# Optimization experiments

Hardware: AMD Instinct MI355X
Metric: run time of the kernel (lower is better)

Reference implementation:

```python
import jax, jax.numpy as jnp
import numpy as np

HEADS = 6
WSIZE = 8
SHIFTS = 4
EPS = 1e-5


def conv1x1(x, w, b=None):
    # x: (B,C,H,W), w: (O,C)
    y = jnp.einsum('bchw,oc->bohw', x, w)
    if b is not None:
        y = y + b[None, :, None, None]
    return y


def spatial_shift(x):
    # ShiftConv2d1 depthwise fixed-kernel conv == per-group spatial shift with zero pad
    C = x.shape[1]
    g = C // 5
    x0, x1, x2, x3, x4 = (x[:, :g], x[:, g:2 * g], x[:, 2 * g:3 * g],
                          x[:, 3 * g:4 * g], x[:, 4 * g:])
    left = jnp.pad(x0[:, :, :, 1:], ((0, 0), (0, 0), (0, 0), (0, 1)))   # kernel (1,2)
    right = jnp.pad(x1[:, :, :, :-1], ((0, 0), (0, 0), (0, 0), (1, 0)))  # kernel (1,0)
    up = jnp.pad(x2[:, :, 1:, :], ((0, 0), (0, 0), (0, 1), (0, 0)))      # kernel (2,1)
    down = jnp.pad(x3[:, :, :-1, :], ((0, 0), (0, 0), (1, 0), (0, 0)))   # kernel (0,1)
    return jnp.concatenate([left, right, up, down, x4], axis=1)


def window_attn(xb, ws, heads, shifts):
    # xb: (B, 2*heads*c, H, W); self-similarity attention q@q^T (no separate K, no scaling)
    if shifts > 0:
        xb = jnp.roll(xb, (-(ws // 2), -(ws // 2)), axis=(2, 3))
    b, c2, H, W = xb.shape
    cd = c2 // (2 * heads)
    nh, nw = H // ws, W // ws
    t = xb.reshape(b, 2, heads, cd, nh, ws, nw, ws)
    t = t.transpose(1, 0, 4, 6, 2, 5, 7, 3).reshape(2, b * nh * nw, heads, ws * ws, cd)
    q, v = t[0], t[1]
    atn = jax.nn.softmax(jnp.einsum('whnc,whmc->whnm', q, q), axis=-1)
    o = jnp.einsum('whnm,whmc->whnc', atn, v)
    o = o.reshape(b, nh, nw, heads, ws, ws, cd)
    o = o.transpose(0, 3, 6, 1, 4, 2, 5).reshape(b, heads * cd, H, W)
    if shifts > 0:
        o = jnp.roll(o, (ws // 2, ws // 2), axis=(2, 3))
    return o


def setup_inputs() -> dict:
    key = jax.random.key(0)
    ks = jax.random.split(key, 8)
    B, C, H, W = 2, 180, 256, 256
    s = 0.05
    return {
        'x': jax.random.normal(ks[0], (B, C, H, W), jnp.float32),
        'w0': jax.random.normal(ks[1], (2 * C, C), jnp.float32) * s,
        'b0': jnp.zeros((2 * C,), jnp.float32),
        'w1': jax.random.normal(ks[2], (C, 2 * C), jnp.float32) * s,
        'b1': jnp.zeros((C,), jnp.float32),
        'w_in': jax.random.normal(ks[3], (2 * C, C), jnp.float32) * s,
        'b_in': jnp.zeros((2 * C,), jnp.float32),
        'bn_g': jnp.ones((2 * C,), jnp.float32),
        'bn_b': jnp.zeros((2 * C,), jnp.float32),
        'w_out': jax.random.normal(ks[4], (C, C), jnp.float32) * s,
        'b_out': jnp.zeros((C,), jnp.float32),
    }


def reference(x, w0, b0, w1, b1, w_in, b_in, bn_g, bn_b, w_out, b_out):
    # --- LFE (shift-conv FFN), exp_ratio=2, relu ---
    y = conv1x1(spatial_shift(x), w0, b0)
    y = jax.nn.relu(y)
    y = conv1x1(spatial_shift(y), w1, b1)
    x = y + x
    # --- GMSA (3 parallel shifted-window self-similarity attentions) ---
    z = conv1x1(x, w_in, b_in)
    mu = z.mean(axis=(0, 2, 3), keepdims=True)
    var = z.var(axis=(0, 2, 3), keepdims=True)  # biased, matching BN training forward
    z = (z - mu) / jnp.sqrt(var + EPS) * bn_g[None, :, None, None] + bn_b[None, :, None, None]
    cs = z.shape[1] // 3
    sizes = [WSIZE // 4, WSIZE // 2, WSIZE]
    outs = [window_attn(z[:, i * cs:(i + 1) * cs], sizes[i], HEADS, SHIFTS)
            for i in range(3)]
    out = conv1x1(jnp.concatenate(outs, axis=1), w_out, b_out)
    return out + x
```

## Files before the change

kernel.cpp:

```cpp
#include <hip/hip_runtime.h>
#include <hip/hip_bf16.h>

#define HWSZ 65536
#define NPIX 131072

typedef unsigned short u16;
typedef __bf16 bf16x8 __attribute__((ext_vector_type(8)));
typedef float f32x4 __attribute__((ext_vector_type(4)));
typedef unsigned short u16x2 __attribute__((ext_vector_type(2)));
typedef unsigned short u16x4 __attribute__((ext_vector_type(4)));
typedef unsigned short u16x8 __attribute__((ext_vector_type(8)));
typedef unsigned short u16x8u __attribute__((ext_vector_type(8), aligned(4)));

__device__ inline u16 f2bf(float f) {
    unsigned int x = __builtin_bit_cast(unsigned int, f);
    unsigned int r = x + 0x7FFFu + ((x >> 16) & 1u);
    return (u16)(r >> 16);
}
__device__ inline float bf2f(u16 u) {
    unsigned int x = ((unsigned int)u) << 16;
    return __builtin_bit_cast(float, x);
}

__global__ __launch_bounds__(256) void prep_w(
    const float* __restrict__ w0, const float* __restrict__ w1,
    const float* __restrict__ wi, const float* __restrict__ wo,
    u16* __restrict__ W0p, u16* __restrict__ W1p,
    u16* __restrict__ Wip, u16* __restrict__ Wop)
{
    const int i = blockIdx.x * 256 + threadIdx.x;
    {
        const int r = i / 192, c = i % 192;
        const bool ok = (r < 360) && (c < 180);
        W0p[i] = ok ? f2bf(w0[r * 180 + c]) : (u16)0;
        Wip[i] = ok ? f2bf(wi[r * 180 + c]) : (u16)0;
    }
    {
        const int r = i / 384, c = i % 384;
        W1p[i] = (r < 180 && c < 360) ? f2bf(w1[r * 360 + c]) : (u16)0;
    }
    if (i < 36864) {
        const int r = i / 192, c = i % 192;
        Wop[i] = (r < 180 && c < 180) ? f2bf(wo[r * 180 + c]) : (u16)0;
    }
}

template<int CI, int CO, int G, int INM, int XSTR, bool RELU, int RES, int OUTM, int OSTR, bool COSPLIT>
__global__ __launch_bounds__(256, 4) void conv_v9(
    const void* __restrict__ Xv, const u16* __restrict__ Wp,
    const float* __restrict__ bias, const void* __restrict__ Rv,
    void* __restrict__ Yv)
{
    constexpr int CI_PAD = ((CI + 31) / 32) * 32;
    constexpr int NSTEP  = CI_PAD / 32;
    constexpr int LDK    = 40;

    __shared__ u16 Xt[2][64 * LDK];

    const int tid = threadIdx.x;
    const int bid = blockIdx.x;
    int px_tile, co0;
    if (COSPLIT) {
        co0     = ((bid >> 3) & 1) * 192;
        px_tile = ((bid >> 4) << 3) | (bid & 7);
    } else {
        co0 = blockIdx.y * 192; px_tile = bid;
    }
    const int p0   = px_tile << 6;
    const int b    = p0 >> 16;
    const int pix0 = p0 & 65535;
    const int h    = pix0 >> 8;
    const int w0c  = pix0 & 255;
    const int lane = tid & 63, wid = tid >> 6;
    const int lr = lane & 15, lg = lane >> 4;
    const int co_wave = co0 + wid * 48;

    const float* Xf = (const float*)Xv + (size_t)b * CI * HWSZ;
    const u16*   Xh = (const u16*)Xv;

    const int xn  = tid & 63;
    const int k4a = tid >> 6;

    auto loadX = [&](int kt, u16x4 (&r)[2]) {
        #pragma unroll
        for (int it = 0; it < 2; ++it) {
            const int k4 = k4a + it * 4;
            const int c0 = kt + k4 * 4;
            u16x4 v = {0, 0, 0, 0};
            if (c0 < CI) {
                int dh = 0, dw = 0;
                if (G > 0) {
                    const int g = c0 / G;
                    if      (g == 0) dw = 1;
                    else if (g == 1) dw = -1;
                    else if (g == 2) dh = 1;
                    else if (g == 3) dh = -1;
                }
                const int hh = h + dh;
                const int wp = w0c + xn + dw;
                if (hh >= 0 && hh < 256 && wp >= 0 && wp < 256) {
                    if constexpr (INM == 1) {
                        v = *(const u16x4*)&Xh[(size_t)((b << 16) | (hh << 8) | wp) * XSTR + c0];
                    } else {
                        const float* xs = Xf + (size_t)c0 * HWSZ + hh * 256 + wp;
                        #pragma unroll
                        for (int j = 0; j < 4; ++j) v[j] = f2bf(xs[(size_t)j * HWSZ]);
                    }
                }
            }
            r[it] = v;
        }
    };

    auto loadW = [&](int kt, bf16x8 (&a)[3]) {
        #pragma unroll
        for (int mf = 0; mf < 3; ++mf)
            a[mf] = *(const bf16x8*)&Wp[(size_t)(co_wave + mf * 16 + lr) * CI_PAD + kt + lg * 8];
    };

    auto writeLDS = [&](u16x4 (&r)[2], int buf) {
        *(u16x4*)&Xt[buf][xn * LDK + k4a * 4]       = r[0];
        *(u16x4*)&Xt[buf][xn * LDK + (k4a + 4) * 4] = r[1];
    };

    f32x4 acc[3][4] = {};
    u16x4 raw[2][2];
    bf16x8 af[2][3];

    loadX(0, raw[0]);
    loadW(0, af[0]);
    writeLDS(raw[0], 0);

    #pragma unroll
    for (int s = 0; s < NSTEP; ++s) {
        const int cur = s & 1, nxt = cur ^ 1;
        __syncthreads();
        if (s + 1 < NSTEP) {
            loadX((s + 1) * 32, raw[nxt]);
            loadW((s + 1) * 32, af[nxt]);
        }
        bf16x8 bfr[4];
        #pragma unroll
        for (int nf = 0; nf < 4; ++nf)
            bfr[nf] = *(const bf16x8*)&Xt[cur][(nf * 16 + lr) * LDK + lg * 8];
        #pragma unroll
        for (int mf = 0; mf < 3; ++mf)
            #pragma unroll
            for (int nf = 0; nf < 4; ++nf)
                acc[mf][nf] = __builtin_amdgcn_mfma_f32_16x16x32_bf16(
                    af[cur][mf], bfr[nf], acc[mf][nf], 0, 0, 0);
        if (s + 1 < NSTEP) writeLDS(raw[nxt], nxt);
    }

    const float* Rf = (const float*)Rv;
    const u16*   Rh = (const u16*)Rv;
    #pragma unroll
    for (int mf = 0; mf < 3; ++mf) {
        const int co_b = co_wave + mf * 16 + lg * 4;
        if (co_b >= CO) continue;
        #pragma unroll
        for (int nf = 0; nf < 4; ++nf) {
            const int pl = pix0 + nf * 16 + lr;
            const size_t pg = (size_t)p0 + nf * 16 + lr;
            float v[4];
            #pragma unroll
            for (int r = 0; r < 4; ++r) {
                v[r] = acc[mf][nf][r] + bias[co_b + r];
                if (RELU) v[r] = fmaxf(v[r], 0.f);
            }
            if (RES == 1) {
                #pragma unroll
                for (int r = 0; r < 4; ++r)
                    v[r] += Rf[((size_t)(b * CO + co_b + r)) * HWSZ + pl];
            }
            if (RES == 2) {
                u16x4 rr = *(const u16x4*)&Rh[pg * 180 + co_b];
                #pragma unroll
                for (int r = 0; r < 4; ++r) v[r] += bf2f(rr[r]);
            }
            if (OUTM == 1) {
                u16x4 o;
                #pragma unroll
                for (int r = 0; r < 4; ++r) o[r] = f2bf(v[r]);
                *(u16x4*)&((u16*)Yv)[pg * OSTR + co_b] = o;
            } else {
                #pragma unroll
                for (int r = 0; r < 4; ++r)
                    ((float*)Yv)[((size_t)(b * CO + co_b + r)) * HWSZ + pl] = v[r];
            }
        }
    }
}

template<int CI, int CO, int G, int XSTR, bool RELU, int RES, int OUTM, int OSTR, bool COSPLIT>
__global__ __launch_bounds__(256) void conv_v10(
    const u16* __restrict__ Xh, const u16* __restrict__ Wp,
    const float* __restrict__ bias, const void* __restrict__ Rv,
    void* __restrict__ Yv)
{
    constexpr int CI_PAD = ((CI + 31) / 32) * 32;
    constexpr int NSTEP  = CI_PAD / 32;

    __shared__ u16 Xt[2][256 * 8];

    const int tid = threadIdx.x;
    const int bid = blockIdx.x;
    int px_tile, co0;
    if (COSPLIT) {
        co0     = ((bid >> 3) & 1) * 192;
        px_tile = ((bid >> 4) << 3) | (bid & 7);
    } else {
        co0 = blockIdx.y * 192; px_tile = bid;
    }
    const int p0   = px_tile << 6;
    const int b    = p0 >> 16;
    const int pix0 = p0 & 65535;
    const int h    = pix0 >> 8;
    const int w0c  = pix0 & 255;
    const int lane = tid & 63, wid = tid >> 6;
    const int lr = lane & 15, lg = lane >> 4;
    const int co_wave = co0 + wid * 48;

    const int sg  = (wid << 6) | lane;
    const int spx = sg >> 2;
    const int khp = sg & 3;
    const int kh  = khp ^ ((spx >> 1) & 3);

    auto stage = [&](int kt, int buf) {
        const int c0 = kt + kh * 8;
        u16* ldst_lane = &Xt[buf][sg * 8];
        int dh = 0, dw = 0; bool uni = true;
        if (G > 0) {
            const int g0 = c0 / G;
            uni = (g0 == (c0 + 7) / G);
            if      (g0 == 0) dw = 1;
            else if (g0 == 1) dw = -1;
            else if (g0 == 2) dh = 1;
            else if (g0 == 3) dh = -1;
        }
        const int hh = h + dh, wp = w0c + spx + dw;
        const bool pxok = (hh >= 0 && hh < 256 && wp >= 0 && wp < 256);
        if (c0 < CI && uni && pxok) {
            const u16* src = &Xh[(size_t)((b << 16) | (hh << 8) | wp) * XSTR + c0];
            u16* wbase = &Xt[buf][(wid << 6) * 8];
            __builtin_amdgcn_global_load_lds(
                (const __attribute__((address_space(1))) unsigned int*)src,
                (__attribute__((address_space(3))) unsigned int*)wbase, 16, 0, 0);
        } else {
            u16x8 t = {0, 0, 0, 0, 0, 0, 0, 0};
            if (c0 < CI && pxok) {
                #pragma unroll
                for (int j = 0; j < 8; ++j) {
                    const int c = c0 + j;
                    if (c < CI) {
                        int dh2 = 0, dw2 = 0;
                        if (G > 0) {
                            const int g = c / G;
                            if      (g == 0) dw2 = 1;
                            else if (g == 1) dw2 = -1;
                            else if (g == 2) dh2 = 1;
                            else if (g == 3) dh2 = -1;
                        }
                        const int h2 = h + dh2, w2 = w0c + spx + dw2;
                        if (h2 >= 0 && h2 < 256 && w2 >= 0 && w2 < 256)
                            t[j] = Xh[(size_t)((b << 16) | (h2 << 8) | w2) * XSTR + c];
                    }
                }
            }
            *(u16x8*)ldst_lane = t;
        }
    };

    auto loadW = [&](int kt, bf16x8 (&a)[3]) {
        #pragma unroll
        for (int mf = 0; mf < 3; ++mf)
            a[mf] = *(const bf16x8*)&Wp[(size_t)(co_wave + mf * 16 + lr) * CI_PAD + kt + lg * 8];
    };

    f32x4 acc[3][4] = {};
    bf16x8 af[2][3];

    stage(0, 0);
    loadW(0, af[0]);
    __syncthreads();

    #pragma unroll
    for (int s = 0; s < NSTEP; ++s) {
        const int cur = s & 1, nxt = cur ^ 1;
        if (s + 1 < NSTEP) {
            stage((s + 1) * 32, nxt);
            loadW((s + 1) * 32, af[nxt]);
        }
        bf16x8 bfr[4];
        #pragma unroll
        for (int nf = 0; nf < 4; ++nf) {
            const int pxr = nf * 16 + lr;
            const int kpp = lg ^ ((pxr >> 1) & 3);
            bfr[nf] = *(const bf16x8*)&Xt[cur][pxr * 32 + kpp * 8];
        }
        #pragma unroll
        for (int mf = 0; mf < 3; ++mf)
            #pragma unroll
            for (int nf = 0; nf < 4; ++nf)
                acc[mf][nf] = __builtin_amdgcn_mfma_f32_16x16x32_bf16(
                    af[cur][mf], bfr[nf], acc[mf][nf], 0, 0, 0);
        __syncthreads();
    }

    const float* Rf = (const float*)Rv;
    const u16*   Rh = (const u16*)Rv;
    #pragma unroll
    for (int mf = 0; mf < 3; ++mf) {
        const int co_b = co_wave + mf * 16 + lg * 4;
        if (co_b >= CO) continue;
        #pragma unroll
        for (int nf = 0; nf < 4; ++nf) {
            const int pl = pix0 + nf * 16 + lr;
            const size_t pg = (size_t)p0 + nf * 16 + lr;
            float v[4];
            #pragma unroll
            for (int r = 0; r < 4; ++r) {
                v[r] = acc[mf][nf][r] + bias[co_b + r];
                if (RELU) v[r] = fmaxf(v[r], 0.f);
            }
            if (RES == 1) {
                #pragma unroll
                for (int r = 0; r < 4; ++r)
                    v[r] += Rf[((size_t)(b * CO + co_b + r)) * HWSZ + pl];
            }
            if (RES == 2) {
                u16x4 rr = *(const u16x4*)&Rh[pg * 180 + co_b];
                #pragma unroll
                for (int r = 0; r < 4; ++r) v[r] += bf2f(rr[r]);
            }
            if (OUTM == 1) {
                u16x4 o;
                #pragma unroll
                for (int r = 0; r < 4; ++r) o[r] = f2bf(v[r]);
                *(u16x4*)&((u16*)Yv)[pg * OSTR + co_b] = o;
            } else {
                #pragma unroll
                for (int r = 0; r < 4; ++r)
                    ((float*)Yv)[((size_t)(b * CO + co_b + r)) * HWSZ + pl] = v[r];
            }
        }
    }
}

__global__ __launch_bounds__(256) void bn_part(const u16* __restrict__ zt,
                                               float* __restrict__ part)
{
    const int tid = threadIdx.x;
    const int oc  = tid & 63;
    const int pp  = tid >> 6;
    if (oc >= 45) return;
    const int stripe = blockIdx.x * 4 + pp;
    const int pb = blockIdx.x * 1024 + pp;
    float s[8] = {}, q[8] = {};
    for (int i = 0; i < 256; ++i) {
        const int p = pb + i * 4;
        u16x8 t = *(const u16x8*)&zt[(size_t)p * 360 + oc * 8];
        #pragma unroll
        for (int j = 0; j < 8; ++j) {
            float v = bf2f(t[j]);
            s[j] += v; q[j] += v * v;
        }
    }
    float* pr = part + ((size_t)stripe * 45 + oc) * 16;
    #pragma unroll
    for (int j = 0; j < 8; ++j) { pr[j] = s[j]; pr[8 + j] = q[j]; }
}

__global__ __launch_bounds__(256) void bn_fin(const float* __restrict__ part,
                                              const float* __restrict__ g,
                                              const float* __restrict__ bb,
                                              float* __restrict__ sc,
                                              float* __restrict__ sh)
{
    const int oc = blockIdx.x;
    const int t  = threadIdx.x;
    const float* p1 = part + ((size_t)t * 45 + oc) * 16;
    const float* p2 = part + ((size_t)(t + 256) * 45 + oc) * 16;
    float v[16];
    #pragma unroll
    for (int k = 0; k < 16; ++k) v[k] = p1[k] + p2[k];
    #pragma unroll
    for (int k = 0; k < 16; ++k)
        for (int m = 32; m; m >>= 1) v[k] += __shfl_xor(v[k], m, 64);
    __shared__ float red[4][16];
    if ((t & 63) == 0) {
        #pragma unroll
        for (int k = 0; k < 16; ++k) red[t >> 6][k] = v[k];
    }
    __syncthreads();
    if (t == 0) {
        const float invN = 1.f / (float)NPIX;
        #pragma unroll
        for (int j = 0; j < 8; ++j) {
            const int c = oc * 8 + j;
            float su = red[0][j] + red[1][j] + red[2][j] + red[3][j];
            float sq = red[0][8+j] + red[1][8+j] + red[2][8+j] + red[3][8+j];
            float mean = su * invN;
            float var  = sq * invN - mean * mean;
            float istd = 1.f / sqrtf(var + 1e-5f);
            float s = g[c] * istd;
            sc[c] = s;
            sh[c] = bb[c] - mean * s;
        }
    }
}

template<int WS>
__global__ __launch_bounds__(256) void attn_v3(
    const u16* __restrict__ zt, const float* __restrict__ scale,
    const float* __restrict__ shiftc, u16* __restrict__ ot, int chunk)
{
    constexpr int NP  = WS * WS;
    constexpr int GPB = 256 / NP;
    constexpr int SH  = WS / 2;
    constexpr int NW  = 256 / WS;

    __shared__ float qs[256 * 12];
    __shared__ float vs[256 * 12];
    __shared__ float scs[120], shs[120];

    const int tid = threadIdx.x;
    if (tid < 120) {
        scs[tid] = scale[chunk * 120 + tid];
        shs[tid] = shiftc[chunk * 120 + tid];
    }

    const int lg  = tid / NP;
    const int n   = tid % NP;
    const int gidx = blockIdx.x * GPB + lg;

    const int head = gidx % 6;
    const int win  = gidx / 6;
    const int wcol = win % NW;
    const int tmp  = win / NW;
    const int wrow = tmp % NW;
    const int b    = tmp / NW;

    const int i = n / WS, j = n % WS;
    const int hh = (wrow * WS + i + SH) & 255;
    const int ww = (wcol * WS + j + SH) & 255;
    const size_t zrow = (size_t)((b << 16) | (hh << 8) | ww) * 360;

    const int cq = chunk * 120 + head * 10;
    const int cl = head * 10;

    u16x8u q8 = *(const u16x8u*)&zt[zrow + cq];
    u16x2  q2 = *(const u16x2*)&zt[zrow + cq + 8];
    u16x8u v8 = *(const u16x8u*)&zt[zrow + cq + 60];
    u16x2  v2 = *(const u16x2*)&zt[zrow + cq + 68];
    __syncthreads();

    float q[10];
    float* qrow = &qs[tid * 12];
    float* vrow = &vs[tid * 12];
    #pragma unroll
    for (int c = 0; c < 8; ++c) {
        q[c] = bf2f(q8[c]) * scs[cl + c] + shs[cl + c];
        qrow[c] = q[c];
        vrow[c] = bf2f(v8[c]) * scs[60 + cl + c] + shs[60 + cl + c];
    }
    q[8] = bf2f(q2[0]) * scs[cl + 8] + shs[cl + 8];
    q[9] = bf2f(q2[1]) * scs[cl + 9] + shs[cl + 9];
    qrow[8] = q[8]; qrow[9] = q[9];
    vrow[8] = bf2f(v2[0]) * scs[60 + cl + 8] + shs[60 + cl + 8];
    vrow[9] = bf2f(v2[1]) * scs[60 + cl + 9] + shs[60 + cl + 9];
    qrow[10] = 0.f; qrow[11] = 0.f;
    vrow[10] = 0.f; vrow[11] = 0.f;
    __syncthreads();

    const float* qg = &qs[(lg * NP) * 12];
    const float* vg = &vs[(lg * NP) * 12];

    float mx = -1e30f;
    for (int m = 0; m < NP; ++m) {
        f32x4 a0 = *(const f32x4*)&qg[m * 12];
        f32x4 a1 = *(const f32x4*)&qg[m * 12 + 4];
        f32x4 a2 = *(const f32x4*)&qg[m * 12 + 8];
        float d = q[0]*a0[0] + q[1]*a0[1] + q[2]*a0[2] + q[3]*a0[3]
                + q[4]*a1[0] + q[5]*a1[1] + q[6]*a1[2] + q[7]*a1[3]
                + q[8]*a2[0] + q[9]*a2[1];
        mx = fmaxf(mx, d);
    }
    float s = 0.f;
    float o[10] = {};
    for (int m = 0; m < NP; ++m) {
        f32x4 a0 = *(const f32x4*)&qg[m * 12];
        f32x4 a1 = *(const f32x4*)&qg[m * 12 + 4];
        f32x4 a2 = *(const f32x4*)&qg[m * 12 + 8];
        float d = q[0]*a0[0] + q[1]*a0[1] + q[2]*a0[2] + q[3]*a0[3]
                + q[4]*a1[0] + q[5]*a1[1] + q[6]*a1[2] + q[7]*a1[3]
                + q[8]*a2[0] + q[9]*a2[1];
        float e = __expf(d - mx);
        s += e;
        f32x4 b0 = *(const f32x4*)&vg[m * 12];
        f32x4 b1 = *(const f32x4*)&vg[m * 12 + 4];
        f32x4 b2 = *(const f32x4*)&vg[m * 12 + 8];
        o[0] += e * b0[0]; o[1] += e * b0[1]; o[2] += e * b0[2]; o[3] += e * b0[3];
        o[4] += e * b1[0]; o[5] += e * b1[1]; o[6] += e * b1[2]; o[7] += e * b1[3];
        o[8] += e * b2[0]; o[9] += e * b2[1];
    }
    const float inv = 1.f / s;
    u16* orow = ot + (size_t)((b << 16) | (hh << 8) | ww) * 180 + chunk * 60 + head * 10;
    u16x8u o8;
    #pragma unroll
    for (int c = 0; c < 8; ++c) o8[c] = f2bf(o[c] * inv);
    u16x2 o2;
    o2[0] = f2bf(o[8] * inv);
    o2[1] = f2bf(o[9] * inv);
    *(u16x8u*)&orow[0] = o8;
    *(u16x2*)&orow[8]  = o2;
}

extern "C" void kernel_launch(void* const* d_in, const int* in_sizes, int n_in,
                              void* d_out, int out_size, void* d_ws, size_t ws_size,
                              hipStream_t stream)
{
    const float* x     = (const float*)d_in[0];
    const float* w0    = (const float*)d_in[1];
    const float* b0    = (const float*)d_in[2];
    const float* w1    = (const float*)d_in[3];
    const float* b1    = (const float*)d_in[4];
    const float* w_in  = (const float*)d_in[5];
    const float* b_in  = (const float*)d_in[6];
    const float* bn_g  = (const float*)d_in[7];
    const float* bn_b  = (const float*)d_in[8];
    const float* w_out = (const float*)d_in[9];
    const float* b_out = (const float*)d_in[10];
    float* out = (float*)d_out;

    u16* y   = (u16*)d_ws;
    u16* x1b = y   + (size_t)NPIX * 360;
    u16* ot  = x1b + (size_t)NPIX * 180;
    u16* W0p = ot  + (size_t)NPIX * 180;
    u16* Wip = W0p + 384 * 192;
    u16* W1p = Wip + 384 * 192;
    u16* Wop = W1p + 192 * 384;
    float* part   = (float*)(Wop + 192 * 192);
    float* scale  = part + 512 * 45 * 16;
    float* shiftc = scale + 360;
    u16* zt = y;

    dim3 blk(256);

    prep_w<<<dim3(288), blk, 0, stream>>>(w0, w1, w_in, w_out, W0p, W1p, Wip, Wop);

    conv_v9<180, 360, 36, 0, 0,   true,  0, 1, 360, false>
        <<<dim3(2048, 2), blk, 0, stream>>>(x, W0p, b0, nullptr, y);
    conv_v10<360, 180, 72, 360, false, 1, 1, 180, false>
        <<<dim3(2048, 1), blk, 0, stream>>>(y, W1p, b1, x, x1b);
    conv_v10<180, 360, 0,  180, false, 0, 1, 360, true>
        <<<dim3(4096), blk, 0, stream>>>(x1b, Wip, b_in, nullptr, zt);
    bn_part<<<dim3(128), blk, 0, stream>>>(zt, part);
    bn_fin<<<dim3(45), blk, 0, stream>>>(part, bn_g, bn_b, scale, shiftc);
    attn_v3<2><<<dim3(3072), blk, 0, stream>>>(zt, scale, shiftc, ot, 0);
    attn_v3<4><<<dim3(3072), blk, 0, stream>>>(zt, scale, shiftc, ot, 1);
    attn_v3<8><<<dim3(3072), blk, 0, stream>>>(zt, scale, shiftc, ot, 2);
    conv_v10<180, 180, 0,  180, false, 2, 0, 0, false>
        <<<dim3(2048, 1), blk, 0, stream>>>(ot, Wop, b_out, x1b, out);
}
```

Before: 408.1 us.

## Use 512-thread blocks covering all 360 output channels in expansion convs

Replaces the conv_v9 kernel, which split the 360 output channels across two blocks, with conv_v14, which uses 512 threads (8 waves) so one block computes all output channels for a 64-pixel tile. It also routes the w_in conv through this kernel instead of conv_v10 with its channel split. The input tile is then loaded and converted once per pixel tile rather than twice, which halves input reads and the fp32-to-bf16 conversion for the first conv. The trade-off is larger blocks and fewer resident blocks, and the output stride is now hardcoded to 360.

```diff
diff --git a/kernel.cpp b/kernel.cpp
--- a/kernel.cpp
+++ b/kernel.cpp
@@ -45,11 +45,10 @@
     }
 }
 
-template<int CI, int CO, int G, int INM, int XSTR, bool RELU, int RES, int OUTM, int OSTR, bool COSPLIT>
-__global__ __launch_bounds__(256, 4) void conv_v9(
+template<int CI, int G, int INM, int XSTR, bool RELU>
+__global__ __launch_bounds__(512) void conv_v14(
     const void* __restrict__ Xv, const u16* __restrict__ Wp,
-    const float* __restrict__ bias, const void* __restrict__ Rv,
-    void* __restrict__ Yv)
+    const float* __restrict__ bias, u16* __restrict__ Yh)
 {
     constexpr int CI_PAD = ((CI + 31) / 32) * 32;
     constexpr int NSTEP  = CI_PAD / 32;
@@ -58,22 +57,14 @@
     __shared__ u16 Xt[2][64 * LDK];
 
     const int tid = threadIdx.x;
-    const int bid = blockIdx.x;
-    int px_tile, co0;
-    if (COSPLIT) {
-        co0     = ((bid >> 3) & 1) * 192;
-        px_tile = ((bid >> 4) << 3) | (bid & 7);
-    } else {
-        co0 = blockIdx.y * 192; px_tile = bid;
-    }
-    const int p0   = px_tile << 6;
+    const int p0   = blockIdx.x << 6;
     const int b    = p0 >> 16;
     const int pix0 = p0 & 65535;
     const int h    = pix0 >> 8;
     const int w0c  = pix0 & 255;
     const int lane = tid & 63, wid = tid >> 6;
     const int lr = lane & 15, lg = lane >> 4;
-    const int co_wave = co0 + wid * 48;
+    const int co_wave = wid * 48;
 
     const float* Xf = (const float*)Xv + (size_t)b * CI * HWSZ;
     const u16*   Xh = (const u16*)Xv;
@@ -81,35 +72,31 @@
     const int xn  = tid & 63;
     const int k4a = tid >> 6;
 
-    auto loadX = [&](int kt, u16x4 (&r)[2]) {
-        #pragma unroll
-        for (int it = 0; it < 2; ++it) {
-            const int k4 = k4a + it * 4;
-            const int c0 = kt + k4 * 4;
-            u16x4 v = {0, 0, 0, 0};
-            if (c0 < CI) {
-                int dh = 0, dw = 0;
-                if (G > 0) {
-                    const int g = c0 / G;
-                    if      (g == 0) dw = 1;
-                    else if (g == 1) dw = -1;
-                    else if (g == 2) dh = 1;
-                    else if (g == 3) dh = -1;
+    auto loadX = [&](int kt, u16x4& r) {
+        const int c0 = kt + k4a * 4;
+        u16x4 v = {0, 0, 0, 0};
+        if (c0 < CI) {
+            int dh = 0, dw = 0;
+            if (G > 0) {
+                const int g = c0 / G;
+                if      (g == 0) dw = 1;
+                else if (g == 1) dw = -1;
+                else if (g == 2) dh = 1;
+                else if (g == 3) dh = -1;
+            }
+            const int hh = h + dh;
+            const int wp = w0c + xn + dw;
+            if (hh >= 0 && hh < 256 && wp >= 0 && wp < 256) {
+                if constexpr (INM == 1) {
+                    v = *(const u16x4*)&Xh[(size_t)((b << 16) | (hh << 8) | wp) * XSTR + c0];
+                } else {
+                    const float* xs = Xf + (size_t)c0 * HWSZ + hh * 256 + wp;
+                    #pragma unroll
+                    for (int j = 0; j < 4; ++j) v[j] = f2bf(xs[(size_t)j * HWSZ]);
                 }
-                const int hh = h + dh;
-                const int wp = w0c + xn + dw;
-                if (hh >= 0 && hh < 256 && wp >= 0 && wp < 256) {
-                    if constexpr (INM == 1) {
-                        v = *(const u16x4*)&Xh[(size_t)((b << 16) | (hh << 8) | wp) * XSTR + c0];
-                    } else {
-                        const float* xs = Xf + (size_t)c0 * HWSZ + hh * 256 + wp;
-                        #pragma unroll
-                        for (int j = 0; j < 4; ++j) v[j] = f2bf(xs[(size_t)j * HWSZ]);
-                    }
-                }
-            }
-            r[it] = v;
-        }
+            }
+        }
+        r = v;
     };
 
     auto loadW = [&](int kt, bf16x8 (&a)[3]) {
@@ -118,13 +105,12 @@
             a[mf] = *(const bf16x8*)&Wp[(size_t)(co_wave + mf * 16 + lr) * CI_PAD + kt + lg * 8];
     };
 
-    auto writeLDS = [&](u16x4 (&r)[2], int buf) {
-        *(u16x4*)&Xt[buf][xn * LDK + k4a * 4]       = r[0];
-        *(u16x4*)&Xt[buf][xn * LDK + (k4a + 4) * 4] = r[1];
+    auto writeLDS = [&](u16x4& r, int buf) {
+        *(u16x4*)&Xt[buf][xn * LDK + k4a * 4] = r;
     };
 
     f32x4 acc[3][4] = {};
-    u16x4 raw[2][2];
+    u16x4 raw[2];
     bf16x8 af[2][3];
 
     loadX(0, raw[0]);
@@ -152,42 +138,21 @@
         if (s + 1 < NSTEP) writeLDS(raw[nxt], nxt);
     }
 
-    const float* Rf = (const float*)Rv;
-    const u16*   Rh = (const u16*)Rv;
     #pragma unroll
     for (int mf = 0; mf < 3; ++mf) {
         const int co_b = co_wave + mf * 16 + lg * 4;
-        if (co_b >= CO) continue;
+        if (co_b >= 360) continue;
         #pragma unroll
         for (int nf = 0; nf < 4; ++nf) {
-            const int pl = pix0 + nf * 16 + lr;
             const size_t pg = (size_t)p0 + nf * 16 + lr;
-            float v[4];
+            u16x4 o;
             #pragma unroll
             for (int r = 0; r < 4; ++r) {
-                v[r] = acc[mf][nf][r] + bias[co_b + r];
-                if (RELU) v[r] = fmaxf(v[r], 0.f);
-            }
-            if (RES == 1) {
-                #pragma unroll
-                for (int r = 0; r < 4; ++r)
-                    v[r] += Rf[((size_t)(b * CO + co_b + r)) * HWSZ + pl];
-            }
-            if (RES == 2) {
-                u16x4 rr = *(const u16x4*)&Rh[pg * 180 + co_b];
-                #pragma unroll
-                for (int r = 0; r < 4; ++r) v[r] += bf2f(rr[r]);
-            }
-            if (OUTM == 1) {
-                u16x4 o;
-                #pragma unroll
-                for (int r = 0; r < 4; ++r) o[r] = f2bf(v[r]);
-                *(u16x4*)&((u16*)Yv)[pg * OSTR + co_b] = o;
-            } else {
-                #pragma unroll
-                for (int r = 0; r < 4; ++r)
-                    ((float*)Yv)[((size_t)(b * CO + co_b + r)) * HWSZ + pl] = v[r];
-            }
+                float v = acc[mf][nf][r] + bias[co_b + r];
+                if (RELU) v = fmaxf(v, 0.f);
+                o[r] = f2bf(v);
+            }
+            *(u16x4*)&Yh[pg * 360 + co_b] = o;
         }
     }
 }
@@ -546,15 +511,16 @@
     u16* zt = y;
 
     dim3 blk(256);
+    dim3 blk8(512);
 
     prep_w<<<dim3(288), blk, 0, stream>>>(w0, w1, w_in, w_out, W0p, W1p, Wip, Wop);
 
-    conv_v9<180, 360, 36, 0, 0,   true,  0, 1, 360, false>
-        <<<dim3(2048, 2), blk, 0, stream>>>(x, W0p, b0, nullptr, y);
+    conv_v14<180, 36, 0, 0,   true >
+        <<<dim3(2048), blk8, 0, stream>>>(x, W0p, b0, y);
     conv_v10<360, 180, 72, 360, false, 1, 1, 180, false>
         <<<dim3(2048, 1), blk, 0, stream>>>(y, W1p, b1, x, x1b);
-    conv_v10<180, 360, 0,  180, false, 0, 1, 360, true>
-        <<<dim3(4096), blk, 0, stream>>>(x1b, Wip, b_in, nullptr, zt);
+    conv_v14<180, 0,  1, 180, false>
+        <<<dim3(2048), blk8, 0, stream>>>(x1b, Wip, b_in, zt);
     bn_part<<<dim3(128), blk, 0, stream>>>(zt, part);
     bn_fin<<<dim3(45), blk, 0, stream>>>(part, bn_g, bn_b, scale, shiftc);
     attn_v3<2><<<dim3(3072), blk, 0, stream>>>(zt, scale, shiftc, ot, 0);
```

Measured after the change: 398.5 us. 2.3% less time.
